# Optimization experiments

Hardware: AMD Instinct MI355X
Metric: run time of the kernel (lower is better)

Reference implementation:

```python
import jax, jax.numpy as jnp
import numpy as np

B, NS, D, H, L, NQ, NK = 32, 4096, 256, 4, 6, 512, 1024
DH = D // H
SCALE = 1.0 / np.sqrt(DH)


def _ln(x, scale, bias, eps=1e-5):
    m = jnp.mean(x, axis=-1, keepdims=True)
    v = jnp.mean((x - m) ** 2, axis=-1, keepdims=True)
    return (x - m) * jax.lax.rsqrt(v + eps) * scale + bias


def setup_inputs() -> dict:
    key = jax.random.key(0)
    ks = jax.random.split(key, 12)
    d = {
        'update_tensor': jax.random.normal(ks[0], (B, NS, D), jnp.float32) * 0.1,
        'emb_table': jax.random.normal(ks[1], (NS + 1, D), jnp.float32) * 0.1,
        'mask_logits': jax.random.uniform(ks[2], (L, NQ, NK), jnp.float32),
        'Wq': jax.random.normal(ks[3], (D, D), jnp.float32) * 0.05,
        'Wk': jax.random.normal(ks[4], (D, D), jnp.float32) * 0.05,
        'Wv': jax.random.normal(ks[5], (D, D), jnp.float32) * 0.05,
        'Wo': jax.random.normal(ks[6], (D, D), jnp.float32) * 0.05,
        'W1': jax.random.normal(ks[7], (D, D), jnp.float32) * 0.05,
        'b1': jnp.zeros((D,), jnp.float32),
        'W2': jax.random.normal(ks[8], (D, D), jnp.float32) * 0.05,
        'b2': jnp.zeros((D,), jnp.float32),
        'sys_scale': jnp.ones((D,), jnp.float32),
        'sys_bias': jnp.zeros((D,), jnp.float32),
        'eff_scale': jnp.ones((D,), jnp.float32),
        'eff_bias': jnp.zeros((D,), jnp.float32),
        'inner_scale': jnp.ones((D,), jnp.float32),
        'inner_bias': jnp.zeros((D,), jnp.float32),
        'outer_scale': jnp.ones((D,), jnp.float32),
        'outer_bias': jnp.zeros((D,), jnp.float32),
        'query_idx': jax.random.randint(ks[9], (L, NQ), 0, NS).astype(jnp.int32),
        'key_idx': jax.random.randint(ks[10], (L, NK), 0, NS).astype(jnp.int32),
    }
    return d


def _hitr(q, k, mask, Wq, Wk, Wv, Wo, W1, b1, W2, b2, in_s, in_b, out_s, out_b):
    # q: [B,NQ,D] (pre-normed), k: [B,NK,D], mask: [NQ,NK] bool
    Q = jnp.einsum('bqd,de->bqe', q, Wq).reshape(B, NQ, H, DH)
    K = jnp.einsum('bkd,de->bke', k, Wk).reshape(B, NK, H, DH)
    V = jnp.einsum('bkd,de->bke', k, Wv).reshape(B, NK, H, DH)
    scores = jnp.einsum('bqhd,bkhd->bhqk', Q, K) * SCALE
    scores = jnp.where(mask[None, None], scores, jnp.float32(-1e9))
    attn = jax.nn.softmax(scores, axis=-1)
    ctx = jnp.einsum('bhqk,bkhd->bqhd', attn, V).reshape(B, NQ, D)
    h = _ln(jnp.einsum('bqd,de->bqe', ctx, Wo), in_s, in_b)
    ffn = jnp.einsum('bqd,de->bqe', jax.nn.gelu(jnp.einsum('bqd,de->bqe', h, W1) + b1), W2) + b2
    return _ln(h + ffn, out_s, out_b)


def reference(update_tensor, emb_table, mask_logits, Wq, Wk, Wv, Wo, W1, b1, W2, b2,
              sys_scale, sys_bias, eff_scale, eff_bias, inner_scale, inner_bias,
              outer_scale, outer_bias, query_idx, key_idx):
    update_result = jnp.zeros_like(update_tensor)
    for l in range(L):  # static hierarchy levels
        qi, ki = query_idx[l], key_idx[l]
        mask = mask_logits[l] > 0.5
        q = _ln(emb_table[qi][None] + update_tensor[:, qi], sys_scale, sys_bias)
        k = _ln(emb_table[ki][None] + update_tensor[:, ki], sys_scale, sys_bias)
        res = _ln(_hitr(q, k, mask, Wq, Wk, Wv, Wo, W1, b1, W2, b2,
                        inner_scale, inner_bias, outer_scale, outer_bias),
                  eff_scale, eff_bias)
        update_tensor = update_tensor.at[:, qi].add(res)
        update_result = update_result.at[:, qi].add(res)
    return update_result
```

## Files before the change

### kernel.cpp

```cpp
#include <hip/hip_runtime.h>
#include <cstdint>
#include <cstddef>

#define B_ 32
#define NS_ 4096
#define D_ 256
#define H_ 4
#define L_ 6
#define NQ_ 512
#define NK_ 1024
#define DH_ 64
#define SCALE_ 0.125f

typedef unsigned short ushort_t;
typedef unsigned long long u64_t;
typedef __bf16 bf16x8 __attribute__((ext_vector_type(8)));
typedef float f32x4 __attribute__((ext_vector_type(4)));

__device__ __forceinline__ ushort_t f2bf(float f) {
  unsigned u = __float_as_uint(f);
  u += 0x7fffu + ((u >> 16) & 1u);
  return (ushort_t)(u >> 16);
}

__device__ __forceinline__ void gld16(const void* g, void* l) {
  __builtin_amdgcn_global_load_lds(
      (__attribute__((address_space(1))) void*)(uintptr_t)g,
      (__attribute__((address_space(3))) void*)(uintptr_t)l, 16, 0, 0);
}

__global__ __launch_bounds__(256) void prep_w(
    const float* __restrict__ w0, const float* __restrict__ w1,
    const float* __restrict__ w2, const float* __restrict__ w3,
    const float* __restrict__ w4, const float* __restrict__ w5,
    ushort_t* __restrict__ wt) {
  const int sel = blockIdx.x >> 8;
  const int n = blockIdx.x & 255;
  const int k = threadIdx.x;
  const float* W = sel == 0 ? w0 : sel == 1 ? w1 : sel == 2 ? w2
                 : sel == 3 ? w3 : sel == 4 ? w4 : w5;
  wt[sel * 65536 + n * 256 + k] = f2bf(W[k * 256 + n]);
}

__global__ __launch_bounds__(256) void prep_mask(
    const float* __restrict__ ml, u64_t* __restrict__ mb) {
  const long gid = (long)blockIdx.x * 256 + threadIdx.x;
  const bool m = ml[gid] > 0.5f;
  const u64_t bal = __ballot(m);
  if ((threadIdx.x & 63) == 0) mb[gid >> 6] = bal;
}

__global__ __launch_bounds__(256) void gather_ln(
    const float* __restrict__ ut, const float* __restrict__ emb,
    const int* __restrict__ qidx, const int* __restrict__ kidx,
    const float* __restrict__ sc, const float* __restrict__ bi,
    ushort_t* __restrict__ qn, ushort_t* __restrict__ kn) {
  const int w = threadIdx.x >> 6, lane = threadIdx.x & 63;
  const int R = blockIdx.x * 4 + w;
  int bb, idx;
  ushort_t* dst;
  long drow;
  if (R < B_ * NQ_) {
    bb = R >> 9; idx = qidx[R & (NQ_ - 1)]; dst = qn; drow = R;
  } else {
    const int r2 = R - B_ * NQ_;
    bb = r2 >> 10; idx = kidx[r2 & (NK_ - 1)]; dst = kn; drow = r2;
  }
  const int c0 = lane * 4;
  const float4 e = *(const float4*)(emb + (long)idx * 256 + c0);
  const float4 u = *(const float4*)(ut + ((long)bb * NS_ + idx) * 256 + c0);
  float x0 = e.x + u.x, x1 = e.y + u.y, x2 = e.z + u.z, x3 = e.w + u.w;
  float s1 = x0 + x1 + x2 + x3;
  float s2 = x0 * x0 + x1 * x1 + x2 * x2 + x3 * x3;
#pragma unroll
  for (int off = 1; off < 64; off <<= 1) {
    s1 += __shfl_xor(s1, off);
    s2 += __shfl_xor(s2, off);
  }
  const float mean = s1 * (1.f / 256.f);
  const float inv = rsqrtf(s2 * (1.f / 256.f) - mean * mean + 1e-5f);
  const float4 scv = *(const float4*)(sc + c0);
  const float4 biv = *(const float4*)(bi + c0);
  ushort4 o;
  o.x = f2bf((x0 - mean) * inv * scv.x + biv.x);
  o.y = f2bf((x1 - mean) * inv * scv.y + biv.y);
  o.z = f2bf((x2 - mean) * inv * scv.z + biv.z);
  o.w = f2bf((x3 - mean) * inv * scv.w + biv.w);
  *(ushort4*)(dst + drow * 256 + c0) = o;
}

template <int EPI>
__device__ __forceinline__ void gemm_body(
    const ushort_t* __restrict__ A, const ushort_t* __restrict__ Bt,
    void* __restrict__ Cout, long m0, int n0, ushort_t* lAB) {
  ushort_t* lA = lAB;
  ushort_t* lB = lAB + 8192;
  const int tid = threadIdx.x;
  const int lane = tid & 63, w = tid >> 6;
  const int quad = lane >> 4, l16 = lane & 15;
  const int wm = w & 1, wn = w >> 1;

  f32x4 acc[4][4] = {};

  for (int kt = 0; kt < 4; ++kt) {
    const int k0 = kt * 64;
#pragma unroll
    for (int p = 0; p < 4; ++p) {
      const int ob = p * 4096 + tid * 16;
      const int row = ob >> 7;
      const int chunk = ((ob >> 4) & 7) ^ (row & 7);
      gld16(A + (m0 + row) * 256 + k0 + chunk * 8, (char*)lA + p * 4096 + w * 1024);
      gld16(Bt + (long)(n0 + row) * 256 + k0 + chunk * 8, (char*)lB + p * 4096 + w * 1024);
    }
    __syncthreads();
#pragma unroll
    for (int ki = 0; ki < 2; ++ki) {
      bf16x8 af[4], bfr[4];
#pragma unroll
      for (int i = 0; i < 4; ++i) {
        const int ra = wm * 64 + i * 16 + l16;
        const int ca = (ki * 4 + quad) ^ (ra & 7);
        af[i] = *(const bf16x8*)&lA[ra * 64 + ca * 8];
        const int rb = wn * 64 + i * 16 + l16;
        const int cb = (ki * 4 + quad) ^ (rb & 7);
        bfr[i] = *(const bf16x8*)&lB[rb * 64 + cb * 8];
      }
#pragma unroll
      for (int mi = 0; mi < 4; ++mi)
#pragma unroll
        for (int ni = 0; ni < 4; ++ni)
          acc[mi][ni] = __builtin_amdgcn_mfma_f32_16x16x32_bf16(af[mi], bfr[ni], acc[mi][ni], 0, 0, 0);
    }
    __syncthreads();
  }

  if (EPI == 4) {
    const long b = m0 >> 10;
    const int kvseg = (int)(m0 & 1023);
#pragma unroll
    for (int hg = 0; hg < 2; ++hg) {
      if (wn == hg) {
#pragma unroll
        for (int mi = 0; mi < 4; ++mi)
#pragma unroll
          for (int ni = 0; ni < 4; ++ni)
#pragma unroll
            for (int r = 0; r < 4; ++r) {
              const int dh = ni * 16 + l16;
              const int kvl = wm * 64 + mi * 16 + quad * 4 + r;
              lAB[dh * 128 + (((kvl >> 3) ^ (dh & 15)) << 3) + (kvl & 7)] =
                  f2bf(acc[mi][ni][r]);
            }
      }
      __syncthreads();
      {
        const int dh = tid >> 2;
        const int head = (n0 >> 6) + hg;
        ushort_t* dst = (ushort_t*)Cout +
            ((b * 4 + head) * 64 + dh) * 1024 + kvseg;
#pragma unroll
        for (int i = 0; i < 4; ++i) {
          const int c = (tid & 3) * 4 + i;
          const int cs = c ^ (dh & 15);
          *(uint4*)(dst + c * 8) = *(const uint4*)&lAB[dh * 128 + cs * 8];
        }
      }
      __syncthreads();
    }
    return;
  }

#pragma unroll
  for (int mi = 0; mi < 4; ++mi) {
#pragma unroll
    for (int ni = 0; ni < 4; ++ni) {
#pragma unroll
      for (int r = 0; r < 4; ++r) {
        const long row = m0 + wm * 64 + mi * 16 + quad * 4 + r;
        const int col = n0 + wn * 64 + ni * 16 + l16;
        float v = acc[mi][ni][r];
        if (EPI == 5) v *= SCALE_;
        ((ushort_t*)Cout)[row * 256 + col] = f2bf(v);
      }
    }
  }
}

__global__ __launch_bounds__(256) void gemm_qkv(
    const ushort_t* __restrict__ qn, const ushort_t* __restrict__ kn,
    const ushort_t* __restrict__ wt,
    ushort_t* __restrict__ Qb, ushort_t* __restrict__ Kb, ushort_t* __restrict__ Vt) {
  __shared__ ushort_t lAB[16384];
  int idx = blockIdx.x;
  if (idx < 256) {
    gemm_body<5>(qn, wt, Qb, (long)(idx & 127) * 128, (idx >> 7) * 128, lAB);
  } else if (idx < 768) {
    idx -= 256;
    gemm_body<0>(kn, wt + 65536, Kb, (long)(idx & 255) * 128, (idx >> 8) * 128, lAB);
  } else {
    idx -= 768;
    gemm_body<4>(kn, wt + 131072, Vt, (long)(idx & 255) * 128, (idx >> 8) * 128, lAB);
  }
}

template <int MODE>
__global__ __launch_bounds__(256) void gemm_band(
    const ushort_t* __restrict__ A, const ushort_t* __restrict__ Bt,
    const float* __restrict__ bias,
    const float* __restrict__ ln1s, const float* __restrict__ ln1b,
    const float* __restrict__ ln2s, const float* __restrict__ ln2b,
    const float* __restrict__ hfres, const int* __restrict__ qidx,
    float* __restrict__ outF, ushort_t* __restrict__ outB,
    float* __restrict__ ut, float* __restrict__ out) {
  __shared__ ushort_t lA[3][2048];
  __shared__ ushort_t lB[3][8192];
  __shared__ float sS1[64][4], sS2[64][4];
  const int tid = threadIdx.x;
  const int lane = tid & 63, w = tid >> 6;
  const int quad = lane >> 4, l16 = lane & 15;
  const long m0 = (long)blockIdx.x * 64;

  auto stage = [&](int kt, int bu) {
    const int k0 = kt * 32;
    {
      const int ob = tid * 16;
      const int row = ob >> 6;
      const int c = (ob >> 4) & 3;
      gld16(A + (m0 + row) * 256 + k0 + (c ^ ((row >> 1) & 3)) * 8,
            (char*)&lA[bu][0] + w * 1024);
    }
#pragma unroll
    for (int p = 0; p < 4; ++p) {
      const int ob = p * 4096 + tid * 16;
      const int row = ob >> 6;
      const int c = (ob >> 4) & 3;
      gld16(Bt + (long)row * 256 + k0 + (c ^ ((row >> 1) & 3)) * 8,
            (char*)&lB[bu][0] + p * 4096 + w * 1024);
    }
  };

  f32x4 acc[4][4] = {};
  stage(0, 0);
  stage(1, 1);
#pragma unroll
  for (int kt = 0; kt < 8; ++kt) {
    const int bu = kt % 3;
    if (kt < 6) stage(kt + 2, (kt + 2) % 3);
    if (kt < 6)       asm volatile("s_waitcnt vmcnt(10)" ::: "memory");
    else if (kt == 6) asm volatile("s_waitcnt vmcnt(5)" ::: "memory");
    else              asm volatile("s_waitcnt vmcnt(0)" ::: "memory");
    __builtin_amdgcn_s_barrier();
    __builtin_amdgcn_sched_barrier(0);
    bf16x8 af[4], bfr[4];
#pragma unroll
    for (int i = 0; i < 4; ++i) {
      const int ra = i * 16 + l16;
      af[i] = *(const bf16x8*)&lA[bu][ra * 32 + ((quad ^ ((ra >> 1) & 3)) * 8)];
      const int rb = w * 64 + i * 16 + l16;
      bfr[i] = *(const bf16x8*)&lB[bu][rb * 32 + ((quad ^ ((rb >> 1) & 3)) * 8)];
    }
#pragma unroll
    for (int mi = 0; mi < 4; ++mi)
#pragma unroll
      for (int ni = 0; ni < 4; ++ni)
        acc[mi][ni] = __builtin_amdgcn_mfma_f32_16x16x32_bf16(af[mi], bfr[ni], acc[mi][ni], 0, 0, 0);
    __builtin_amdgcn_sched_barrier(0);
    __builtin_amdgcn_s_barrier();
  }

  if (MODE == 2) {
    float bcol[4];
#pragma unroll
    for (int ni = 0; ni < 4; ++ni) bcol[ni] = bias[w * 64 + ni * 16 + l16];
#pragma unroll
    for (int mi = 0; mi < 4; ++mi)
#pragma unroll
      for (int r = 0; r < 4; ++r) {
        const long row = m0 + mi * 16 + quad * 4 + r;
#pragma unroll
        for (int ni = 0; ni < 4; ++ni) {
          float v = acc[mi][ni][r] + bcol[ni];
          const float u = 0.7978845608028654f * (v + 0.044715f * v * v * v);
          v = 0.5f * v * (1.0f + tanhf(u));
          outB[row * 256 + (w * 64 + ni * 16 + l16)] = f2bf(v);
        }
      }
    return;
  }

  if (MODE == 6) {
#pragma unroll
    for (int mi = 0; mi < 4; ++mi)
#pragma unroll
      for (int r = 0; r < 4; ++r) {
        float a1 = 0.f, a2 = 0.f;
#pragma unroll
        for (int ni = 0; ni < 4; ++ni) {
          const float v = acc[mi][ni][r];
          a1 += v; a2 += v * v;
        }
#pragma unroll
        for (int off = 1; off < 16; off <<= 1) {
          a1 += __shfl_xor(a1, off);
          a2 += __shfl_xor(a2, off);
        }
        if (l16 == 0) {
          sS1[mi * 16 + quad * 4 + r][w] = a1;
          sS2[mi * 16 + quad * 4 + r][w] = a2;
        }
      }
    __syncthreads();
    float l1sv[4], l1bv[4];
#pragma unroll
    for (int ni = 0; ni < 4; ++ni) {
      const int col = w * 64 + ni * 16 + l16;
      l1sv[ni] = ln1s[col]; l1bv[ni] = ln1b[col];
    }
#pragma unroll
    for (int mi = 0; mi < 4; ++mi)
#pragma unroll
      for (int r = 0; r < 4; ++r) {
        const int rowi = mi * 16 + quad * 4 + r;
        const f32x4 v1 = *(const f32x4*)&sS1[rowi][0];
        const f32x4 v2 = *(const f32x4*)&sS2[rowi][0];
        const float s1 = v1[0] + v1[1] + v1[2] + v1[3];
        const float s2 = v2[0] + v2[1] + v2[2] + v2[3];
        const float mean = s1 * (1.f / 256.f);
        const float inv = rsqrtf(s2 * (1.f / 256.f) - mean * mean + 1e-5f);
        const long row = m0 + rowi;
#pragma unroll
        for (int ni = 0; ni < 4; ++ni) {
          const int col = w * 64 + ni * 16 + l16;
          const float y = (acc[mi][ni][r] - mean) * inv * l1sv[ni] + l1bv[ni];
          outF[row * 256 + col] = y;
          outB[row * 256 + col] = f2bf(y);
        }
      }
    return;
  }

  {
    float bcol[4], l1sv[4], l1bv[4], l2sv[4], l2bv[4];
#pragma unroll
    for (int ni = 0; ni < 4; ++ni) {
      const int col = w * 64 + ni * 16 + l16;
      bcol[ni] = bias[col];
      l1sv[ni] = ln1s[col]; l1bv[ni] = ln1b[col];
      l2sv[ni] = ln2s[col]; l2bv[ni] = ln2b[col];
    }
#pragma unroll
    for (int mi = 0; mi < 4; ++mi)
#pragma unroll
      for (int r = 0; r < 4; ++r) {
        const long row = m0 + mi * 16 + quad * 4 + r;
        float a1 = 0.f, a2 = 0.f;
#pragma unroll
        for (int ni = 0; ni < 4; ++ni) {
          const int col = w * 64 + ni * 16 + l16;
          const float v = acc[mi][ni][r] + bcol[ni] + hfres[row * 256 + col];
          acc[mi][ni][r] = v;
          a1 += v; a2 += v * v;
        }
#pragma unroll
        for (int off = 1; off < 16; off <<= 1) {
          a1 += __shfl_xor(a1, off);
          a2 += __shfl_xor(a2, off);
        }
        if (l16 == 0) {
          sS1[mi * 16 + quad * 4 + r][w] = a1;
          sS2[mi * 16 + quad * 4 + r][w] = a2;
        }
      }
    __syncthreads();
    float py1[4][4], py2[4][4];
#pragma unroll
    for (int mi = 0; mi < 4; ++mi)
#pragma unroll
      for (int r = 0; r < 4; ++r) {
        const int rowi = mi * 16 + quad * 4 + r;
        const f32x4 v1 = *(const f32x4*)&sS1[rowi][0];
        const f32x4 v2 = *(const f32x4*)&sS2[rowi][0];
        const float s1 = v1[0] + v1[1] + v1[2] + v1[3];
        const float s2 = v2[0] + v2[1] + v2[2] + v2[3];
        const float mean = s1 * (1.f / 256.f);
        const float inv = rsqrtf(s2 * (1.f / 256.f) - mean * mean + 1e-5f);
        float a1 = 0.f, a2 = 0.f;
#pragma unroll
        for (int ni = 0; ni < 4; ++ni) {
          const float y = (acc[mi][ni][r] - mean) * inv * l1sv[ni] + l1bv[ni];
          acc[mi][ni][r] = y;
          a1 += y; a2 += y * y;
        }
        py1[mi][r] = a1; py2[mi][r] = a2;
      }
    __syncthreads();
#pragma unroll
    for (int mi = 0; mi < 4; ++mi)
#pragma unroll
      for (int r = 0; r < 4; ++r) {
        float a1 = py1[mi][r], a2 = py2[mi][r];
#pragma unroll
        for (int off = 1; off < 16; off <<= 1) {
          a1 += __shfl_xor(a1, off);
          a2 += __shfl_xor(a2, off);
        }
        if (l16 == 0) {
          sS1[mi * 16 + quad * 4 + r][w] = a1;
          sS2[mi * 16 + quad * 4 + r][w] = a2;
        }
      }
    __syncthreads();
#pragma unroll
    for (int mi = 0; mi < 4; ++mi)
#pragma unroll
      for (int r = 0; r < 4; ++r) {
        const int rowi = mi * 16 + quad * 4 + r;
        const f32x4 v1 = *(const f32x4*)&sS1[rowi][0];
        const f32x4 v2 = *(const f32x4*)&sS2[rowi][0];
        const float s1 = v1[0] + v1[1] + v1[2] + v1[3];
        const float s2 = v2[0] + v2[1] + v2[2] + v2[3];
        const float mean = s1 * (1.f / 256.f);
        const float inv = rsqrtf(s2 * (1.f / 256.f) - mean * mean + 1e-5f);
        const long row = m0 + rowi;
        const int idx = qidx[(int)(row & (NQ_ - 1))];
        const long base = ((row >> 9) * (long)NS_ + idx) * 256;
#pragma unroll
        for (int ni = 0; ni < 4; ++ni) {
          const int col = w * 64 + ni * 16 + l16;
          const float z = (acc[mi][ni][r] - mean) * inv * l2sv[ni] + l2bv[ni];
          atomicAdd(&ut[base + col], z);
          atomicAdd(&out[base + col], z);
        }
      }
  }
}

__global__ __launch_bounds__(256) void attn_kernel(
    const ushort_t* __restrict__ Qb, const ushort_t* __restrict__ Kb,
    const ushort_t* __restrict__ Vt, const u64_t* __restrict__ mbits,
    ushort_t* __restrict__ ctx) {
  __shared__ ushort_t lQ[4096], lK[4096], lVt[4096], lP[4096];
  const int tid = threadIdx.x;
  const int lane = tid & 63, w = tid >> 6;
  const int quad = lane >> 4, l16 = lane & 15;
  const int bid = blockIdx.x;
  const int qt = bid >> 7, pair = bid & 127;
  const int h = pair & 3, b = pair >> 2;
  const int q0 = qt * 64;
  const long qrow0 = (long)b * NQ_ + q0;
  const long krow0 = (long)b * NK_;
  const ushort_t* vbase = Vt + ((long)pair * 64) * 1024;
  const u64_t* mrow = mbits + (long)(q0 + w * 16 + quad * 4) * (NK_ / 64);

#pragma unroll
  for (int p = 0; p < 2; ++p) {
    const int ob = p * 4096 + tid * 16;
    const int row = ob >> 7;
    const int chunk = ((ob >> 4) & 7) ^ (row & 7);
    gld16(Qb + (qrow0 + row) * 256 + h * 64 + chunk * 8, (char*)lQ + p * 4096 + w * 1024);
    gld16(Kb + (krow0 + row) * 256 + h * 64 + chunk * 8, (char*)lK + p * 4096 + w * 1024);
  }

  f32x4 o_acc[4] = {};
  f32x4 l_acc = {};
  bf16x8 ones;
#pragma unroll
  for (int i = 0; i < 8; ++i) ones[i] = (__bf16)1.0f;

  u64_t wd[4];
#pragma unroll
  for (int r = 0; r < 4; ++r) wd[r] = mrow[r << 4];

  for (int kt = 0; kt < 16; ++kt) {
    __syncthreads();

#pragma unroll
    for (int p = 0; p < 2; ++p) {
      const int ob = p * 4096 + tid * 16;
      const int row = ob >> 7;
      const int chunk = ((ob >> 4) & 7) ^ (row & 7);
      gld16(vbase + (long)row * 1024 + kt * 64 + chunk * 8,
            (char*)lVt + p * 4096 + w * 1024);
    }

    f32x4 s[4] = {};
    __builtin_amdgcn_s_setprio(1);
#pragma unroll
    for (int ki = 0; ki < 2; ++ki) {
      const int rq = w * 16 + l16;
      const int cq = (ki * 4 + quad) ^ (rq & 7);
      const bf16x8 qf = *(const bf16x8*)&lQ[rq * 64 + cq * 8];
#pragma unroll
      for (int ni = 0; ni < 4; ++ni) {
        const int rk = ni * 16 + l16;
        const int ck = (ki * 4 + quad) ^ (rk & 7);
        const bf16x8 kf = *(const bf16x8*)&lK[rk * 64 + ck * 8];
        s[ni] = __builtin_amdgcn_mfma_f32_16x16x32_bf16(qf, kf, s[ni], 0, 0, 0);
      }
    }
    __builtin_amdgcn_s_setprio(0);

    u64_t wdn[4];
    if (kt < 15) {
#pragma unroll
      for (int r = 0; r < 4; ++r) wdn[r] = mrow[(r << 4) + kt + 1];
    }

#pragma unroll
    for (int r = 0; r < 4; ++r) {
      const int rowp = w * 16 + quad * 4 + r;
#pragma unroll
      for (int ni = 0; ni < 4; ++ni) {
        const bool keep = (wd[r] >> (ni * 16 + l16)) & 1ull;
        const float pv = keep ? __expf(s[ni][r]) : 0.f;
        const int col = ni * 16 + l16;
        lP[rowp * 64 + (((col >> 3) ^ (rowp & 7)) << 3) + (col & 7)] = f2bf(pv);
      }
    }
    if (kt < 15) {
#pragma unroll
      for (int r = 0; r < 4; ++r) wd[r] = wdn[r];
    }

    __syncthreads();

    if (kt < 15) {
#pragma unroll
      for (int p = 0; p < 2; ++p) {
        const int ob = p * 4096 + tid * 16;
        const int row = ob >> 7;
        const int chunk = ((ob >> 4) & 7) ^ (row & 7);
        gld16(Kb + (krow0 + (kt + 1) * 64 + row) * 256 + h * 64 + chunk * 8,
              (char*)lK + p * 4096 + w * 1024);
      }
    }

    __builtin_amdgcn_s_setprio(1);
#pragma unroll
    for (int ki = 0; ki < 2; ++ki) {
      const int rp = w * 16 + l16;
      const int cp = (ki * 4 + quad) ^ (rp & 7);
      const bf16x8 pf = *(const bf16x8*)&lP[rp * 64 + cp * 8];
      l_acc = __builtin_amdgcn_mfma_f32_16x16x32_bf16(pf, ones, l_acc, 0, 0, 0);
#pragma unroll
      for (int ni = 0; ni < 4; ++ni) {
        const int rv = ni * 16 + l16;
        const int cv = (ki * 4 + quad) ^ (rv & 7);
        const bf16x8 vf = *(const bf16x8*)&lVt[rv * 64 + cv * 8];
        o_acc[ni] = __builtin_amdgcn_mfma_f32_16x16x32_bf16(pf, vf, o_acc[ni], 0, 0, 0);
      }
    }
    __builtin_amdgcn_s_setprio(0);
  }

#pragma unroll
  for (int r = 0; r < 4; ++r) {
    const float inv = 1.0f / l_acc[r];
    const long rowg = qrow0 + w * 16 + quad * 4 + r;
#pragma unroll
    for (int ni = 0; ni < 4; ++ni) {
      const int col = h * 64 + ni * 16 + l16;
      ctx[rowg * 256 + col] = f2bf(o_acc[ni][r] * inv);
    }
  }
}

extern "C" void kernel_launch(void* const* d_in, const int* in_sizes, int n_in,
                              void* d_out, int out_size, void* d_ws, size_t ws_size,
                              hipStream_t stream) {
  float* ut = (float*)d_in[0];
  const float* emb = (const float*)d_in[1];
  const float* maskl = (const float*)d_in[2];
  const float* Wq = (const float*)d_in[3];
  const float* Wk = (const float*)d_in[4];
  const float* Wv = (const float*)d_in[5];
  const float* Wo = (const float*)d_in[6];
  const float* W1 = (const float*)d_in[7];
  const float* b1 = (const float*)d_in[8];
  const float* W2 = (const float*)d_in[9];
  const float* b2 = (const float*)d_in[10];
  const float* sys_s = (const float*)d_in[11];
  const float* sys_b = (const float*)d_in[12];
  const float* eff_s = (const float*)d_in[13];
  const float* eff_b = (const float*)d_in[14];
  const float* in_s = (const float*)d_in[15];
  const float* in_b = (const float*)d_in[16];
  const float* out_s = (const float*)d_in[17];
  const float* out_b = (const float*)d_in[18];
  const int* qidx = (const int*)d_in[19];
  const int* kidx = (const int*)d_in[20];
  float* out = (float*)d_out;

  char* p = (char*)d_ws;
  auto carve = [&](size_t bytes) {
    void* r = (void*)p;
    p += (bytes + 255) & ~(size_t)255;
    return r;
  };
  ushort_t* wt = (ushort_t*)carve((size_t)6 * 65536 * 2);
  u64_t* mb = (u64_t*)carve((size_t)L_ * NQ_ * (NK_ / 64) * 8);
  ushort_t* qn = (ushort_t*)carve((size_t)16384 * 256 * 2);
  ushort_t* kn = (ushort_t*)carve((size_t)32768 * 256 * 2);
  ushort_t* Qb = (ushort_t*)carve((size_t)16384 * 256 * 2);
  ushort_t* Kb = (ushort_t*)carve((size_t)32768 * 256 * 2);
  ushort_t* Vt = (ushort_t*)carve((size_t)32768 * 256 * 2);

  ushort_t* ctx = qn;
  ushort_t* g = Qb;
  ushort_t* hb = Kb;
  float* hf = (float*)Vt;

  hipMemsetAsync(d_out, 0, (size_t)out_size, stream);
  prep_w<<<1536, 256, 0, stream>>>(Wq, Wk, Wv, Wo, W1, W2, wt);
  prep_mask<<<(L_ * NQ_ * NK_) / 256, 256, 0, stream>>>(maskl, mb);

  for (int l = 0; l < L_; ++l) {
    gather_ln<<<B_ * (NQ_ + NK_) / 4, 256, 0, stream>>>(
        ut, emb, qidx + l * NQ_, kidx + l * NK_, sys_s, sys_b, qn, kn);
    gemm_qkv<<<1280, 256, 0, stream>>>(qn, kn, wt, Qb, Kb, Vt);
    attn_kernel<<<1024, 256, 0, stream>>>(
        Qb, Kb, Vt, mb + (size_t)l * NQ_ * (NK_ / 64), ctx);
    gemm_band<6><<<256, 256, 0, stream>>>(
        ctx, wt + 3 * 65536, nullptr, in_s, in_b, nullptr, nullptr,
        nullptr, nullptr, hf, hb, nullptr, nullptr);
    gemm_band<2><<<256, 256, 0, stream>>>(
        hb, wt + 4 * 65536, b1, nullptr, nullptr, nullptr, nullptr,
        nullptr, nullptr, nullptr, g, nullptr, nullptr);
    gemm_band<7><<<256, 256, 0, stream>>>(
        g, wt + 5 * 65536, b2, out_s, out_b, eff_s, eff_b,
        hf, qidx + l * NQ_, nullptr, nullptr, ut, out);
  }
}
```

Measured before the change: 1.261 ms.

## Triple-buffer K/V tiles in attention kernel and stage mask bits in LDS

The attention kernel now keeps three LDS buffers for K and V tiles and prefetches two tiles ahead, using explicit vmcnt waits and raw s_barrier instead of __syncthreads around each stage. The per-block mask bitwords are loaded once into LDS up front rather than read from global memory every iteration. This aims to hide global-load latency behind MFMA work and drop a synchronization point per iteration. In exchange it uses more LDS per block, which may reduce occupancy, and it relies on hand-counted vmcnt values being correct.

```diff
diff --git a/kernel.cpp b/kernel.cpp
--- a/kernel.cpp
+++ b/kernel.cpp
@@ -439,7 +439,11 @@
     const ushort_t* __restrict__ Qb, const ushort_t* __restrict__ Kb,
     const ushort_t* __restrict__ Vt, const u64_t* __restrict__ mbits,
     ushort_t* __restrict__ ctx) {
-  __shared__ ushort_t lQ[4096], lK[4096], lVt[4096], lP[4096];
+  __shared__ ushort_t lQ[4096];
+  __shared__ ushort_t lK[3][4096];
+  __shared__ ushort_t lVt[3][4096];
+  __shared__ ushort_t lP[4096];
+  __shared__ u64_t lM[1024];
   const int tid = threadIdx.x;
   const int lane = tid & 63, w = tid >> 6;
   const int quad = lane >> 4, l16 = lane & 15;
@@ -450,7 +454,6 @@
   const long qrow0 = (long)b * NQ_ + q0;
   const long krow0 = (long)b * NK_;
   const ushort_t* vbase = Vt + ((long)pair * 64) * 1024;
-  const u64_t* mrow = mbits + (long)(q0 + w * 16 + quad * 4) * (NK_ / 64);
 
 #pragma unroll
   for (int p = 0; p < 2; ++p) {
@@ -458,30 +461,43 @@
     const int row = ob >> 7;
     const int chunk = ((ob >> 4) & 7) ^ (row & 7);
     gld16(Qb + (qrow0 + row) * 256 + h * 64 + chunk * 8, (char*)lQ + p * 4096 + w * 1024);
-    gld16(Kb + (krow0 + row) * 256 + h * 64 + chunk * 8, (char*)lK + p * 4096 + w * 1024);
-  }
-
-  f32x4 o_acc[4] = {};
-  f32x4 l_acc = {};
-  bf16x8 ones;
-#pragma unroll
-  for (int i = 0; i < 8; ++i) ones[i] = (__bf16)1.0f;
-
-  u64_t wd[4];
-#pragma unroll
-  for (int r = 0; r < 4; ++r) wd[r] = mrow[r << 4];
-
-  for (int kt = 0; kt < 16; ++kt) {
-    __syncthreads();
-
+    gld16((const char*)(mbits + (long)q0 * 16) + ob, (char*)lM + p * 4096 + w * 1024);
+  }
+
+  auto stageKV = [&](int kt, int bu) {
 #pragma unroll
     for (int p = 0; p < 2; ++p) {
       const int ob = p * 4096 + tid * 16;
       const int row = ob >> 7;
       const int chunk = ((ob >> 4) & 7) ^ (row & 7);
+      gld16(Kb + (krow0 + kt * 64 + row) * 256 + h * 64 + chunk * 8,
+            (char*)&lK[bu][0] + p * 4096 + w * 1024);
       gld16(vbase + (long)row * 1024 + kt * 64 + chunk * 8,
-            (char*)lVt + p * 4096 + w * 1024);
-    }
+            (char*)&lVt[bu][0] + p * 4096 + w * 1024);
+    }
+  };
+
+  f32x4 o_acc[4] = {};
+  f32x4 l_acc = {};
+  bf16x8 ones;
+#pragma unroll
+  for (int i = 0; i < 8; ++i) ones[i] = (__bf16)1.0f;
+
+  stageKV(0, 0);
+  stageKV(1, 1);
+
+  for (int kt = 0; kt < 16; ++kt) {
+    const int bu = kt % 3;
+    if (kt < 14) stageKV(kt + 2, (kt + 2) % 3);
+    if (kt < 14)       asm volatile("s_waitcnt vmcnt(8)" ::: "memory");
+    else if (kt == 14) asm volatile("s_waitcnt vmcnt(4)" ::: "memory");
+    else               asm volatile("s_waitcnt vmcnt(0)" ::: "memory");
+    __builtin_amdgcn_s_barrier();
+    __builtin_amdgcn_sched_barrier(0);
+
+    u64_t wd[4];
+#pragma unroll
+    for (int r = 0; r < 4; ++r) wd[r] = lM[(w * 16 + quad * 4 + r) * 16 + kt];
 
     f32x4 s[4] = {};
     __builtin_amdgcn_s_setprio(1);
@@ -494,17 +510,11 @@
       for (int ni = 0; ni < 4; ++ni) {
         const int rk = ni * 16 + l16;
         const int ck = (ki * 4 + quad) ^ (rk & 7);
-        const bf16x8 kf = *(const bf16x8*)&lK[rk * 64 + ck * 8];
+        const bf16x8 kf = *(const bf16x8*)&lK[bu][rk * 64 + ck * 8];
         s[ni] = __builtin_amdgcn_mfma_f32_16x16x32_bf16(qf, kf, s[ni], 0, 0, 0);
       }
     }
     __builtin_amdgcn_s_setprio(0);
-
-    u64_t wdn[4];
-    if (kt < 15) {
-#pragma unroll
-      for (int r = 0; r < 4; ++r) wdn[r] = mrow[(r << 4) + kt + 1];
-    }
 
 #pragma unroll
     for (int r = 0; r < 4; ++r) {
@@ -517,23 +527,6 @@
         lP[rowp * 64 + (((col >> 3) ^ (rowp & 7)) << 3) + (col & 7)] = f2bf(pv);
       }
     }
-    if (kt < 15) {
-#pragma unroll
-      for (int r = 0; r < 4; ++r) wd[r] = wdn[r];
-    }
-
-    __syncthreads();
-
-    if (kt < 15) {
-#pragma unroll
-      for (int p = 0; p < 2; ++p) {
-        const int ob = p * 4096 + tid * 16;
-        const int row = ob >> 7;
-        const int chunk = ((ob >> 4) & 7) ^ (row & 7);
-        gld16(Kb + (krow0 + (kt + 1) * 64 + row) * 256 + h * 64 + chunk * 8,
-              (char*)lK + p * 4096 + w * 1024);
-      }
-    }
 
     __builtin_amdgcn_s_setprio(1);
 #pragma unroll
@@ -546,11 +539,13 @@
       for (int ni = 0; ni < 4; ++ni) {
         const int rv = ni * 16 + l16;
         const int cv = (ki * 4 + quad) ^ (rv & 7);
-        const bf16x8 vf = *(const bf16x8*)&lVt[rv * 64 + cv * 8];
+        const bf16x8 vf = *(const bf16x8*)&lVt[bu][rv * 64 + cv * 8];
         o_acc[ni] = __builtin_amdgcn_mfma_f32_16x16x32_bf16(pf, vf, o_acc[ni], 0, 0, 0);
       }
     }
     __builtin_amdgcn_s_setprio(0);
+    __builtin_amdgcn_sched_barrier(0);
+    __builtin_amdgcn_s_barrier();
   }
 
 #pragma unroll
```

New measurement: 1.748 ms. +38.6%, slower.
